# Performance work log

Hardware: AMD Instinct MI355X
Metric: run time of the kernel (lower is better)

The kernel has to match this reference:

```python
import jax, jax.numpy as jnp
import numpy as np

B = 256          # batch of images
TOK = 256        # 16x16 tokens per image
V = 1024         # codebook size
D = 256          # code dim


def setup_inputs() -> dict:
    key = jax.random.key(0)
    k1, k2, k3, k4 = jax.random.split(key, 4)
    image_seq = jax.random.randint(k1, (B, TOK), 0, V, dtype=jnp.int64)
    image_seq2 = jax.random.randint(k2, (B, TOK), 0, V, dtype=jnp.int64)
    alpha = jax.random.uniform(k3, (1,), dtype=jnp.float32)
    W = jax.random.normal(k4, (V, D), dtype=jnp.float32)
    return {"image_seq": image_seq, "image_seq2": image_seq2, "alpha": alpha, "W": W}


def reference(image_seq, image_seq2, alpha, W):
    a = alpha[0]
    # gather codebook entries: [B, TOK, D]
    emb = W[image_seq]
    emb2 = W[image_seq2]
    x = (1.0 - a) * emb + a * emb2
    xf = x.reshape(-1, D)                        # [N, D], N = B*TOK
    # brute-force L2 distance to every code, without materializing [N, V, D]:
    d = (jnp.sum(xf * xf, axis=-1, keepdims=True)
         - 2.0 * xf @ W.T
         + jnp.sum(W * W, axis=-1)[None, :])
    idx = jnp.argmin(d, axis=1)                  # top-1 nearest code, [N]
    # get_codebook_entry: gather, reshape to bhwc, permute to bchw
    z_q = W[idx].reshape(B, 16, 16, D)           # [B, 16, 16, 256]
    z_q = jnp.transpose(z_q, (0, 3, 1, 2))       # [B, 256, 16, 16]
    return z_q
```

## Files before the change

kernel.cpp:

```cpp
#include <hip/hip_runtime.h>

static constexpr int Vn = 1024;
static constexpr int Dn = 256;
static constexpr int NT = 65536;

__global__ __launch_bounds__(256) void gram_kernel(const float* __restrict__ W,
                                                   float* __restrict__ G,
                                                   float* __restrict__ norms) {
    __shared__ float As[32][33];
    __shared__ float Bs[32][33];
    const int tid = threadIdx.x;
    const int tx = tid & 15;
    const int ty = tid >> 4;
    const int bm = blockIdx.y * 32;
    const int bn = blockIdx.x * 32;
    float acc[2][2] = {};
    for (int k0 = 0; k0 < Dn; k0 += 32) {
#pragma unroll
        for (int s = 0; s < 4; ++s) {
            const int e = tid + 256 * s;
            const int m = e >> 5;
            const int k = e & 31;
            As[k][m] = W[(bm + m) * Dn + k0 + k];
            Bs[k][m] = W[(bn + m) * Dn + k0 + k];
        }
        __syncthreads();
#pragma unroll
        for (int kk = 0; kk < 32; ++kk) {
            float a[2], b[2];
#pragma unroll
            for (int u = 0; u < 2; ++u) a[u] = As[kk][ty + 16 * u];
#pragma unroll
            for (int w = 0; w < 2; ++w) b[w] = Bs[kk][tx + 16 * w];
#pragma unroll
            for (int u = 0; u < 2; ++u)
#pragma unroll
                for (int w = 0; w < 2; ++w)
                    acc[u][w] = fmaf(a[u], b[w], acc[u][w]);
        }
        __syncthreads();
    }
#pragma unroll
    for (int u = 0; u < 2; ++u) {
        const int row = bm + ty + 16 * u;
#pragma unroll
        for (int w = 0; w < 2; ++w) {
            const int col = bn + tx + 16 * w;
            G[row * Vn + col] = acc[u][w];
            if (row == col) norms[row] = acc[u][w];
        }
    }
}

__global__ __launch_bounds__(256) void argmin_kernel(const int* __restrict__ seq,
                                                     const int* __restrict__ seq2,
                                                     const float* __restrict__ alpha,
                                                     const float* __restrict__ G,
                                                     const float* __restrict__ norms,
                                                     int* __restrict__ out_idx) {
    __shared__ float nrm[Vn];
    const int tid = threadIdx.x;
    {
        ((float4*)nrm)[tid] = ((const float4*)norms)[tid];
    }
    __syncthreads();
    const float a = alpha[0];
    const float c0 = -2.0f * (1.0f - a);
    const float c1 = -2.0f * a;
    const int wave = tid >> 6;
    const int lane = tid & 63;
    const int base_t = blockIdx.x * 16 + wave * 4;
    const float4* nr = (const float4*)nrm;
    int iv[4], jv[4];
#pragma unroll
    for (int q = 0; q < 4; ++q) { iv[q] = seq[base_t + q]; jv[q] = seq2[base_t + q]; }
#pragma unroll
    for (int pair = 0; pair < 2; ++pair) {
        const int qa = pair * 2, qb = pair * 2 + 1;
        const float4* GiA = (const float4*)(G + iv[qa] * Vn);
        const float4* GjA = (const float4*)(G + jv[qa] * Vn);
        const float4* GiB = (const float4*)(G + iv[qb] * Vn);
        const float4* GjB = (const float4*)(G + jv[qb] * Vn);
        float4 gia[4], gja[4], gib[4], gjb[4];
#pragma unroll
        for (int s = 0; s < 4; ++s) {
            const int e = s * 64 + lane;
            gia[s] = GiA[e];
            gja[s] = GjA[e];
            gib[s] = GiB[e];
            gjb[s] = GjB[e];
        }
        float bestA = __builtin_inff(), bestB = __builtin_inff();
        int vA = 0, vB = 0;
#pragma unroll
        for (int s = 0; s < 4; ++s) {
            const int e = s * 64 + lane;
            const float4 nn = nr[e];
            const int v = e * 4;
            {
                const float s0 = fmaf(c1, gja[s].x, fmaf(c0, gia[s].x, nn.x));
                const float s1 = fmaf(c1, gja[s].y, fmaf(c0, gia[s].y, nn.y));
                const float s2 = fmaf(c1, gja[s].z, fmaf(c0, gia[s].z, nn.z));
                const float s3 = fmaf(c1, gja[s].w, fmaf(c0, gia[s].w, nn.w));
                if (s0 < bestA) { bestA = s0; vA = v; }
                if (s1 < bestA) { bestA = s1; vA = v + 1; }
                if (s2 < bestA) { bestA = s2; vA = v + 2; }
                if (s3 < bestA) { bestA = s3; vA = v + 3; }
            }
            {
                const float s0 = fmaf(c1, gjb[s].x, fmaf(c0, gib[s].x, nn.x));
                const float s1 = fmaf(c1, gjb[s].y, fmaf(c0, gib[s].y, nn.y));
                const float s2 = fmaf(c1, gjb[s].z, fmaf(c0, gib[s].z, nn.z));
                const float s3 = fmaf(c1, gjb[s].w, fmaf(c0, gib[s].w, nn.w));
                if (s0 < bestB) { bestB = s0; vB = v; }
                if (s1 < bestB) { bestB = s1; vB = v + 1; }
                if (s2 < bestB) { bestB = s2; vB = v + 2; }
                if (s3 < bestB) { bestB = s3; vB = v + 3; }
            }
        }
#pragma unroll
        for (int off = 32; off >= 1; off >>= 1) {
            const float oa = __shfl_down(bestA, off, 64);
            const int   va = __shfl_down(vA, off, 64);
            if (oa < bestA || (oa == bestA && va < vA)) { bestA = oa; vA = va; }
            const float ob = __shfl_down(bestB, off, 64);
            const int   vb = __shfl_down(vB, off, 64);
            if (ob < bestB || (ob == bestB && vb < vB)) { bestB = ob; vB = vb; }
        }
        if (lane == 0) {
            out_idx[base_t + qa] = vA;
            out_idx[base_t + qb] = vB;
        }
    }
}

__global__ __launch_bounds__(256) void gather_transpose_kernel(const float* __restrict__ W,
                                                               const int* __restrict__ idx,
                                                               float* __restrict__ out) {
    __shared__ float tile[64][65];
    const int b   = blockIdx.z;
    const int hw0 = blockIdx.x * 64;
    const int d0  = blockIdx.y * 64;
    const int tx  = threadIdx.x & 63;
    const int ty  = threadIdx.x >> 6;
#pragma unroll
    for (int r = ty; r < 64; r += 4) {
        const int row = idx[b * 256 + hw0 + r];
        tile[r][tx] = W[row * Dn + d0 + tx];
    }
    __syncthreads();
#pragma unroll
    for (int r = ty; r < 64; r += 4) {
        out[b * 65536 + (d0 + r) * 256 + hw0 + tx] = tile[tx][r];
    }
}

extern "C" void kernel_launch(void* const* d_in, const int* in_sizes, int n_in,
                              void* d_out, int out_size, void* d_ws, size_t ws_size,
                              hipStream_t stream) {
    const int*   seq   = (const int*)d_in[0];
    const int*   seq2  = (const int*)d_in[1];
    const float* alpha = (const float*)d_in[2];
    const float* W     = (const float*)d_in[3];
    float* out = (float*)d_out;

    char* ws = (char*)d_ws;
    float* G     = (float*)(ws);
    float* norms = (float*)(ws + 4194304);
    int*   idx   = (int*)  (ws + 4198400);

    gram_kernel<<<dim3(32, 32), 256, 0, stream>>>(W, G, norms);
    argmin_kernel<<<NT / 16, 256, 0, stream>>>(seq, seq2, alpha, G, norms, idx);
    gather_transpose_kernel<<<dim3(4, 4, 256), 256, 0, stream>>>(W, idx, out);
}
```

Baseline: 142.9 us.

## Fuse argmin with codebook gather and transposed output write

```diff
diff --git a/kernel.cpp b/kernel.cpp
--- a/kernel.cpp
+++ b/kernel.cpp
@@ -52,13 +52,16 @@
     }
 }
 
-__global__ __launch_bounds__(256) void argmin_kernel(const int* __restrict__ seq,
-                                                     const int* __restrict__ seq2,
-                                                     const float* __restrict__ alpha,
-                                                     const float* __restrict__ G,
-                                                     const float* __restrict__ norms,
-                                                     int* __restrict__ out_idx) {
+__global__ __launch_bounds__(256) void argmin_write_kernel(const int* __restrict__ seq,
+                                                           const int* __restrict__ seq2,
+                                                           const float* __restrict__ alpha,
+                                                           const float* __restrict__ G,
+                                                           const float* __restrict__ norms,
+                                                           const float* __restrict__ W,
+                                                           float* __restrict__ out) {
     __shared__ float nrm[Vn];
+    __shared__ float T[32][257];
+    __shared__ int bestVs[32];
     const int tid = threadIdx.x;
     {
         ((float4*)nrm)[tid] = ((const float4*)norms)[tid];
@@ -69,89 +72,99 @@
     const float c1 = -2.0f * a;
     const int wave = tid >> 6;
     const int lane = tid & 63;
-    const int base_t = blockIdx.x * 16 + wave * 4;
+    const int t0 = blockIdx.x * 32;
     const float4* nr = (const float4*)nrm;
-    int iv[4], jv[4];
+
+    for (int bb = 0; bb < 2; ++bb) {
+        const int base_t = t0 + wave * 8 + bb * 4;
+        const int base_l = wave * 8 + bb * 4;
+        int iv[4], jv[4];
 #pragma unroll
-    for (int q = 0; q < 4; ++q) { iv[q] = seq[base_t + q]; jv[q] = seq2[base_t + q]; }
+        for (int q = 0; q < 4; ++q) { iv[q] = seq[base_t + q]; jv[q] = seq2[base_t + q]; }
 #pragma unroll
-    for (int pair = 0; pair < 2; ++pair) {
-        const int qa = pair * 2, qb = pair * 2 + 1;
-        const float4* GiA = (const float4*)(G + iv[qa] * Vn);
-        const float4* GjA = (const float4*)(G + jv[qa] * Vn);
-        const float4* GiB = (const float4*)(G + iv[qb] * Vn);
-        const float4* GjB = (const float4*)(G + jv[qb] * Vn);
-        float4 gia[4], gja[4], gib[4], gjb[4];
+        for (int pair = 0; pair < 2; ++pair) {
+            const int qa = pair * 2, qb = pair * 2 + 1;
+            const float4* GiA = (const float4*)(G + iv[qa] * Vn);
+            const float4* GjA = (const float4*)(G + jv[qa] * Vn);
+            const float4* GiB = (const float4*)(G + iv[qb] * Vn);
+            const float4* GjB = (const float4*)(G + jv[qb] * Vn);
+            float4 gia[4], gja[4], gib[4], gjb[4];
 #pragma unroll
-        for (int s = 0; s < 4; ++s) {
-            const int e = s * 64 + lane;
-            gia[s] = GiA[e];
-            gja[s] = GjA[e];
-            gib[s] = GiB[e];
-            gjb[s] = GjB[e];
-        }
-        float bestA = __builtin_inff(), bestB = __builtin_inff();
-        int vA = 0, vB = 0;
+            for (int s = 0; s < 4; ++s) {
+                const int e = s * 64 + lane;
+                gia[s] = GiA[e];
+                gja[s] = GjA[e];
+                gib[s] = GiB[e];
+                gjb[s] = GjB[e];
+            }
+            float bestA = __builtin_inff(), bestB = __builtin_inff();
+            int vA = 0, vB = 0;
 #pragma unroll
-        for (int s = 0; s < 4; ++s) {
-            const int e = s * 64 + lane;
-            const float4 nn = nr[e];
-            const int v = e * 4;
-            {
-                const float s0 = fmaf(c1, gja[s].x, fmaf(c0, gia[s].x, nn.x));
-                const float s1 = fmaf(c1, gja[s].y, fmaf(c0, gia[s].y, nn.y));
-                const float s2 = fmaf(c1, gja[s].z, fmaf(c0, gia[s].z, nn.z));
-                const float s3 = fmaf(c1, gja[s].w, fmaf(c0, gia[s].w, nn.w));
-                if (s0 < bestA) { bestA = s0; vA = v; }
-                if (s1 < bestA) { bestA = s1; vA = v + 1; }
-                if (s2 < bestA) { bestA = s2; vA = v + 2; }
-                if (s3 < bestA) { bestA = s3; vA = v + 3; }
+            for (int s = 0; s < 4; ++s) {
+                const int e = s * 64 + lane;
+                const float4 nn = nr[e];
+                const int v = e * 4;
+                {
+                    const float s0 = fmaf(c1, gja[s].x, fmaf(c0, gia[s].x, nn.x));
+                    const float s1 = fmaf(c1, gja[s].y, fmaf(c0, gia[s].y, nn.y));
+                    const float s2 = fmaf(c1, gja[s].z, fmaf(c0, gia[s].z, nn.z));
+                    const float s3 = fmaf(c1, gja[s].w, fmaf(c0, gia[s].w, nn.w));
+                    if (s0 < bestA) { bestA = s0; vA = v; }
+                    if (s1 < bestA) { bestA = s1; vA = v + 1; }
+                    if (s2 < bestA) { bestA = s2; vA = v + 2; }
+                    if (s3 < bestA) { bestA = s3; vA = v + 3; }
+                }
+                {
+                    const float s0 = fmaf(c1, gjb[s].x, fmaf(c0, gib[s].x, nn.x));
+                    const float s1 = fmaf(c1, gjb[s].y, fmaf(c0, gib[s].y, nn.y));
+                    const float s2 = fmaf(c1, gjb[s].z, fmaf(c0, gib[s].z, nn.z));
+                    const float s3 = fmaf(c1, gjb[s].w, fmaf(c0, gib[s].w, nn.w));
+                    if (s0 < bestB) { bestB = s0; vB = v; }
+                    if (s1 < bestB) { bestB = s1; vB = v + 1; }
+                    if (s2 < bestB) { bestB = s2; vB = v + 2; }
+                    if (s3 < bestB) { bestB = s3; vB = v + 3; }
+                }
             }
-            {
-                const float s0 = fmaf(c1, gjb[s].x, fmaf(c0, gib[s].x, nn.x));
-                const float s1 = fmaf(c1, gjb[s].y, fmaf(c0, gib[s].y, nn.y));
-                const float s2 = fmaf(c1, gjb[s].z, fmaf(c0, gib[s].z, nn.z));
-                const float s3 = fmaf(c1, gjb[s].w, fmaf(c0, gib[s].w, nn.w));
-                if (s0 < bestB) { bestB = s0; vB = v; }
-                if (s1 < bestB) { bestB = s1; vB = v + 1; }
-                if (s2 < bestB) { bestB = s2; vB = v + 2; }
-                if (s3 < bestB) { bestB = s3; vB = v + 3; }
+#pragma unroll
+            for (int off = 32; off >= 1; off >>= 1) {
+                const float oa = __shfl_down(bestA, off, 64);
+                const int   va = __shfl_down(vA, off, 64);
+                if (oa < bestA || (oa == bestA && va < vA)) { bestA = oa; vA = va; }
+                const float ob = __shfl_down(bestB, off, 64);
+                const int   vb = __shfl_down(vB, off, 64);
+                if (ob < bestB || (ob == bestB && vb < vB)) { bestB = ob; vB = vb; }
+            }
+            if (lane == 0) {
+                bestVs[base_l + qa] = vA;
+                bestVs[base_l + qb] = vB;
             }
         }
+    }
+    __syncthreads();
+
+    const int l16 = tid & 15;
 #pragma unroll
-        for (int off = 32; off >= 1; off >>= 1) {
-            const float oa = __shfl_down(bestA, off, 64);
-            const int   va = __shfl_down(vA, off, 64);
-            if (oa < bestA || (oa == bestA && va < vA)) { bestA = oa; vA = va; }
-            const float ob = __shfl_down(bestB, off, 64);
-            const int   vb = __shfl_down(vB, off, 64);
-            if (ob < bestB || (ob == bestB && vb < vB)) { bestB = ob; vB = vb; }
-        }
-        if (lane == 0) {
-            out_idx[base_t + qa] = vA;
-            out_idx[base_t + qb] = vB;
+    for (int half = 0; half < 2; ++half) {
+        const int tok = half * 16 + (tid >> 4);
+        const int v = bestVs[tok];
+        const float4* Wr = (const float4*)(W + v * Dn);
+#pragma unroll
+        for (int p = 0; p < 4; ++p) {
+            const int d4 = p * 16 + l16;
+            *(float4*)(&T[tok][d4 * 4]) = Wr[d4];
         }
     }
-}
+    __syncthreads();
 
-__global__ __launch_bounds__(256) void gather_transpose_kernel(const float* __restrict__ W,
-                                                               const int* __restrict__ idx,
-                                                               float* __restrict__ out) {
-    __shared__ float tile[64][65];
-    const int b   = blockIdx.z;
-    const int hw0 = blockIdx.x * 64;
-    const int d0  = blockIdx.y * 64;
-    const int tx  = threadIdx.x & 63;
-    const int ty  = threadIdx.x >> 6;
+    const int b   = t0 >> 8;
+    const int hw0 = t0 & 255;
+    float* outb = out + b * 65536 + hw0;
+    const int hw = tid & 31;
+    const int dofs = tid >> 5;
 #pragma unroll
-    for (int r = ty; r < 64; r += 4) {
-        const int row = idx[b * 256 + hw0 + r];
-        tile[r][tx] = W[row * Dn + d0 + tx];
-    }
-    __syncthreads();
-#pragma unroll
-    for (int r = ty; r < 64; r += 4) {
-        out[b * 65536 + (d0 + r) * 256 + hw0 + tx] = tile[tx][r];
+    for (int dp = 0; dp < 256; dp += 8) {
+        const int d = dp + dofs;
+        __builtin_nontemporal_store(T[hw][d], outb + d * 256 + hw);
     }
 }
 
@@ -167,9 +180,7 @@
     char* ws = (char*)d_ws;
     float* G     = (float*)(ws);
     float* norms = (float*)(ws + 4194304);
-    int*   idx   = (int*)  (ws + 4198400);
 
     gram_kernel<<<dim3(32, 32), 256, 0, stream>>>(W, G, norms);
-    argmin_kernel<<<NT / 16, 256, 0, stream>>>(seq, seq2, alpha, G, norms, idx);
-    gather_transpose_kernel<<<dim3(4, 4, 256), 256, 0, stream>>>(W, idx, out);
+    argmin_write_kernel<<<NT / 32, 256, 0, stream>>>(seq, seq2, alpha, G, norms, W, out);
 }
```

Measured after the change: 136.6 us. 1.05x faster.
